# Performance work log

Hardware: AMD Instinct MI355X
Metric: run time of the kernel (lower is better)

## Reference

```python
import jax, jax.numpy as jnp
import numpy as np

SCALE = 64 ** -0.5
MAX_LR = 0.01


def newtonschulz5(t, steps=5, eps=1e-7, coefs=(3.4445, -4.775, 2.0315)):
    # t: [h, i, j]; orthogonalize via quintic Newton-Schulz iteration
    a, b, c = coefs
    should_transpose = t.shape[-2] > t.shape[-1]
    if should_transpose:
        t = jnp.swapaxes(t, -1, -2)
    norm = jnp.sqrt(jnp.sum(t * t, axis=(-1, -2), keepdims=True))
    t = t / jnp.maximum(norm, eps)
    for _ in range(steps):
        A = t @ jnp.swapaxes(t, -1, -2)
        B = b * A + c * (A @ A)
        t = a * t + B @ t
    if should_transpose:
        t = jnp.swapaxes(t, -1, -2)
    return t


def setup_inputs() -> dict:
    key = jax.random.key(0)
    ks = jax.random.split(key, 7)
    b, n, d, h, dh = 2, 2048, 512, 8, 64
    s = 0.05  # scale random weights for numerical sanity (softmax not one-hot)
    return {
        "tokens": jax.random.normal(ks[0], (b, n, d), jnp.float32),
        "rms_weight": jnp.ones((d,), jnp.float32),
        "wq": jax.random.normal(ks[1], (h, d, dh), jnp.float32) * s,
        "wk": jax.random.normal(ks[2], (h, d, dh), jnp.float32) * s,
        "wv": jax.random.normal(ks[3], (h, d, dh), jnp.float32) * s,
        "wo": jax.random.normal(ks[4], (h, dh, d), jnp.float32) * s,
        "lr_w": jax.random.normal(ks[5], (1, d), jnp.float32) * s,
        "tv_w": jax.random.normal(ks[6], (d, d), jnp.float32) * s,
        "return_next_memories": 1,
    }


def reference(tokens, rms_weight, wq, wk, wv, wo, lr_w, tv_w, return_next_memories):
    eps = jnp.finfo(tokens.dtype).eps
    # RMSNorm (torch nn.RMSNorm with eps=None -> finfo eps)
    t = tokens * jax.lax.rsqrt(jnp.mean(tokens * tokens, axis=-1, keepdims=True) + eps) * rms_weight

    q = jnp.einsum('bnd,hde->bhne', t, wq)  # [b,h,n,dh]
    k = jnp.einsum('bnd,hde->bhne', t, wk)
    v = jnp.einsum('bnd,hde->bhne', t, wv)

    score = jnp.einsum('bhie,bhje->bhij', q, k) * SCALE
    n = score.shape[-1]
    causal_mask = jnp.triu(jnp.ones((n, n), bool), 1)
    score = jnp.where(causal_mask, -jnp.finfo(score.dtype).max, score)
    attn = jax.nn.softmax(score, axis=-1)
    out = jnp.einsum('bhij,bhje->bhie', attn, v)  # [b,h,n,dh]
    pred_values = jnp.einsum('bhne,hed->bnd', out, wo)

    if not return_next_memories:
        return pred_values

    # target values: Linear(dim,dim,no bias) + LayerNorm(no affine) on shifted tokens
    tv = jnp.einsum('bnd,od->bno', t[:, 1:], tv_w)
    mu = jnp.mean(tv, axis=-1, keepdims=True)
    var = jnp.var(tv, axis=-1, keepdims=True)
    target_values = (tv - mu) * jax.lax.rsqrt(var + 1e-5)

    tok = t[:, :-1]                       # [b,n-1,d]
    pred_fw = pred_values[:, :-1]
    out_t = out[:, :, :-1]
    attn_t = attn[:, :, :-1, :-1]
    q_t, k_t, v_t = q[:, :, :-1], k[:, :, :-1], v[:, :, :-1]

    lr = jax.nn.sigmoid(jnp.einsum('bnd,od->bno', tok, lr_w)) * MAX_LR  # [b,n-1,1]
    error = (target_values - pred_fw) * lr

    dout = jnp.einsum('bnd,hed->bhne', error, wo)            # [b,h,n-1,dh]
    dwo = jnp.einsum('bnd,bhne->hed', error, out_t)          # [h,dh,d]
    delta = jnp.sum(dout * out_t, axis=-1, keepdims=True)    # [b,h,n-1,1]
    dv = jnp.einsum('bhij,bhie->bhje', attn_t, dout)
    dattn = jnp.einsum('bhje,bhie->bhij', v_t, dout)
    dscore = SCALE * attn_t * (dattn - delta)
    dq = jnp.einsum('bhje,bhij->bhie', k_t, dscore)
    dk = jnp.einsum('bhie,bhij->bhje', q_t, dscore)
    dwq = jnp.einsum('bhie,bid->hde', dq, tok)
    dwk = jnp.einsum('bhje,bjd->hde', dk, tok)
    dwv = jnp.einsum('bhje,bjd->hde', dv, tok)

    # muon update: Newton-Schulz orthogonalization of value/output fast-weight grads
    dwv = newtonschulz5(dwv)
    dwo = newtonschulz5(dwo)

    return (pred_values, dwq, dwk, dwv, dwo)
```

## Files before the change

### kernel.cpp

```cpp
#include <hip/hip_runtime.h>
#include <float.h>
#include <math.h>

#define B_   2
#define N_   2048
#define D_   512
#define H_   8
#define DH_  64
#define NM_  2047
#define SCALE_F 0.125f
#define LBK 72

typedef __attribute__((ext_vector_type(8))) short bf16x8;
typedef __attribute__((ext_vector_type(4))) float f32x4;
#define MFMA_B16(a,b,c) __builtin_amdgcn_mfma_f32_16x16x32_bf16(a,b,c,0,0,0)

__device__ __forceinline__ short f2bf(float f){
  unsigned u = __float_as_uint(f);
  unsigned r = u + 0x7fffu + ((u>>16)&1u);
  return (short)(r>>16);
}
__device__ __forceinline__ float bf2f(short s){
  return __uint_as_float(((unsigned)(unsigned short)s)<<16);
}
// ... 348 lines not shown
  s1=wred64(s1); s2=wred64(s2); s3=wred64(s3);
  __shared__ float r1[4],r2[4],r3[4];
  if((tid&63)==0){ int w=tid>>6; r1[w]=s1; r2[w]=s2; r3[w]=s3; }
  __syncthreads();
  float S1=r1[0]+r1[1]+r1[2]+r1[3];
  float S2=r2[0]+r2[1]+r2[2]+r2[3];
  float S3=r3[0]+r3[1]+r3[2]+r3[3];
  float mu  = S1*(1.f/512.f);
  float var = S2*(1.f/512.f) - mu*mu;
  float rstd= rsqrtf(var + 1e-5f);
  float lr  = 0.01f/(1.f+__expf(-S3));
  tv[tid]     = ((v0-mu)*rstd - pr[tid])*lr;
  tv[tid+256] = ((v1-mu)*rstd - pr[tid+256])*lr;
}

__global__ __launch_bounds__(256) void k_gemm_dout(const short* __restrict__ erb,
    const short* __restrict__ wob, short* __restrict__ doh, short* __restrict__ dot){
  __shared__ __attribute__((aligned(16))) short as[64][LBK], bs[64][LBK];
  int r0=blockIdx.x<<6, h=blockIdx.y;
  f32x4 acc[4];
  #pragma unroll
  for(int nb=0;nb<4;nb++) acc[nb]=(f32x4){0.f,0.f,0.f,0.f};
  gemm64(erb+(size_t)r0*512, 512, wob+(size_t)h*32768, 512, 8, as, bs, acc);
  int tid=threadIdx.x, w=tid>>6, lane=tid&63, lg=lane>>4, ln=lane&15;
  size_t bh=(size_t)(r0>>11)*8+h;
  int n0=(r0&2047)+w*16+lg*4;
  #pragma unroll
  for(int nb=0;nb<4;nb++){
    int e=nb*16+ln;
    short4 s4;
    s4.x=f2bf(acc[nb][0]); s4.y=f2bf(acc[nb][1]);
    s4.z=f2bf(acc[nb][2]); s4.w=f2bf(acc[nb][3]);
    doh[(bh*2048+n0  )*64+e]=s4.x;
    doh[(bh*2048+n0+1)*64+e]=s4.y;
    doh[(bh*2048+n0+2)*64+e]=s4.z;
    doh[(bh*2048+n0+3)*64+e]=s4.w;
    *(short4*)&dot[(bh*64+e)*2048+n0]=s4;
  }
}

__global__ __launch_bounds__(256) void k_delta(const short* __restrict__ doh,
    const short* __restrict__ obb, float* __restrict__ delta){
  int rid = blockIdx.x*4 + (threadIdx.x>>6);
  int lane = threadIdx.x&63;
  if(rid >= B_*H_*NM_) return;
  int b = rid/(H_*NM_); int rem = rid - b*H_*NM_;
  int h = rem/NM_; int i = rem - h*NM_;
  float v = bf2f(doh[((size_t)(b*H_+h)*N_ + i)*DH_ + lane])
          * bf2f(obb[((size_t)(b*N_+i))*D_ + h*DH_ + lane]);
  v = wred64(v);
  if(lane==0) delta[((size_t)(b*H_+h))*N_ + i] = v;
}

__global__ __launch_bounds__(256) void k_fa_dq(const short* __restrict__ qh,
    const short* __restrict__ kh, const short* __restrict__ vh,
    const short* __restrict__ kt, const short* __restrict__ doh,
    const float* __restrict__ lse, const float* __restrict__ delta,
    short* __restrict__ dqt, short* __restrict__ dqp1){
  int bh = blockIdx.x, it = blockIdx.y, half = blockIdx.z;
  int i0 = it<<6;
  const short* qhb = qh + (size_t)bh*N_*DH_;
  const short* khb = kh + (size_t)bh*N_*DH_;
  const short* vhb = vh + (size_t)bh*N_*DH_;
  const short* ktb = kt + (size_t)bh*DH_*N_;
  const short* dohb= doh+ (size_t)bh*N_*DH_;
  __shared__ __attribute__((aligned(16))) short ks[64][LBK], vs[64][LBK], kts[64][LBK];
  __shared__ __attribute__((aligned(16))) short psb[4][16][LBK];
  int tid=threadIdx.x, w=tid>>6, lane=tid&63, lg=lane>>4, ln=lane&15;
  bf16x8 aq[2], ad[2];
  float Lr[4], dl[4];
  #pragma unroll
  for(int s=0;s<2;s++){
    aq[s]=*(const bf16x8*)&qhb[(size_t)(i0+w*16+ln)*DH_+32*s+lg*8];
    ad[s]=*(const bf16x8*)&dohb[(size_t)(i0+w*16+ln)*DH_+32*s+lg*8];
  }
  #pragma unroll
  for(int r=0;r<4;r++){
    int ii=i0+w*16+lg*4+r;
    Lr[r]=lse[(size_t)bh*N_+ii];
    dl[r]=(ii<NM_)?delta[(size_t)bh*N_+ii]:0.f;
  }
  f32x4 acc[4];
  #pragma unroll
  for(int nb=0;nb<4;nb++) acc[nb]=(f32x4){0.f,0.f,0.f,0.f};
  int4 ka0,ka1,va0,va1,ta0,ta1;
  tload(khb+(size_t)half*64*DH_, DH_, tid, ka0,ka1);
  tload(vhb+(size_t)half*64*DH_, DH_, tid, va0,va1);
  tload(ktb+half*64, N_, tid, ta0,ta1);
  for(int jt=half;jt<=it;jt+=2){
    int j0=jt<<6;
    bool msk_needed = (jt==it) || (it==31);
    __syncthreads();
    twrite(ks, tid, ka0,ka1);
    twrite(vs, tid, va0,va1);
    twrite(kts, tid, ta0,ta1);
    if(jt+2<=it){
      tload(khb+(size_t)(jt+2)*64*DH_, DH_, tid, ka0,ka1);
      tload(vhb+(size_t)(jt+2)*64*DH_, DH_, tid, va0,va1);
      tload(ktb+(jt+2)*64, N_, tid, ta0,ta1);
    }
    __syncthreads();
    f32x4 sv[4], dav[4];
    __builtin_amdgcn_s_setprio(1);
    #pragma unroll
    for(int nb=0;nb<4;nb++){
      f32x4 z={0.f,0.f,0.f,0.f}, zd={0.f,0.f,0.f,0.f};
      #pragma unroll
      for(int s=0;s<2;s++){
        bf16x8 bk=*(const bf16x8*)&ks[nb*16+ln][32*s+lg*8];
        bf16x8 bv=*(const bf16x8*)&vs[nb*16+ln][32*s+lg*8];
        z = MFMA_B16(aq[s], bk, z);
        zd= MFMA_B16(ad[s], bv, zd);
      }
      sv[nb]=z; dav[nb]=zd;
    }
    __builtin_amdgcn_s_setprio(0);
    if(msk_needed){
      #pragma unroll
      for(int r=0;r<4;r++){
        int ii=i0+w*16+lg*4+r;
        #pragma unroll
        for(int nb=0;nb<4;nb++){
          int jj=j0+nb*16+ln;
          float pv=__expf(sv[nb][r]*SCALE_F - Lr[r]);
          float dsv=SCALE_F*pv*(dav[nb][r]-dl[r]);
          if(jj>ii || ii>=NM_ || jj>=NM_) dsv=0.f;
          psb[w][lg*4+r][ln+16*nb]=f2bf(dsv);
        }
      }
    } else {
      #pragma unroll
      for(int r=0;r<4;r++)
        #pragma unroll
        for(int nb=0;nb<4;nb++){
          float pv=__expf(sv[nb][r]*SCALE_F - Lr[r]);
          psb[w][lg*4+r][ln+16*nb]=f2bf(SCALE_F*pv*(dav[nb][r]-dl[r]));
        }
    }
    lds_fence();
    __builtin_amdgcn_s_setprio(1);
    #pragma unroll
    for(int nb=0;nb<4;nb++){
      #pragma unroll
      for(int s=0;s<2;s++){
        bf16x8 pa = *(const bf16x8*)&psb[w][ln][32*s+lg*8];
        bf16x8 bk = *(const bf16x8*)&kts[nb*16+ln][32*s+lg*8];
        acc[nb]=MFMA_B16(pa,bk,acc[nb]);
      }
    }
    __builtin_amdgcn_s_setprio(0);
    lds_fence();
  }
  short* dst = half? dqp1 : dqt;
  #pragma unroll
  for(int nb=0;nb<4;nb++){
    short4 s4;
    s4.x=f2bf(acc[nb][0]); s4.y=f2bf(acc[nb][1]);
    s4.z=f2bf(acc[nb][2]); s4.w=f2bf(acc[nb][3]);
    *(short4*)&dst[((size_t)bh*64 + nb*16+ln)*2048 + i0+w*16+lg*4]=s4;
  }
}

__global__ __launch_bounds__(256) void k_dqred(short* __restrict__ dqt,
    const short* __restrict__ dqp1){
  size_t i = ((size_t)blockIdx.x*256 + threadIdx.x)*8;
  int4 a = *(const int4*)&dqt[i];
  int4 b = *(const int4*)&dqp1[i];
  short* pa=(short*)&a; const short* pb=(const short*)&b;
  short out[8];
  #pragma unroll
  for(int k=0;k<8;k++) out[k]=f2bf(bf2f(pa[k])+bf2f(pb[k]));
  *(int4*)&dqt[i] = *(int4*)out;
}

__global__ __launch_bounds__(256) void k_fa_dkv(const short* __restrict__ kh,
    const short* __restrict__ vh, const short* __restrict__ qh,
    const short* __restrict__ qt, const short* __restrict__ doh,
    const short* __restrict__ dot,
    const float* __restrict__ lse, const float* __restrict__ delta,
    short* __restrict__ dkt, short* __restrict__ dvt,
    short* __restrict__ dkp1, short* __restrict__ dvp1){
  int bh = blockIdx.x, jt = blockIdx.y, half = blockIdx.z;
  int j0 = jt<<6;
  const short* khb = kh + (size_t)bh*N_*DH_;
  const short* vhb = vh + (size_t)bh*N_*DH_;
  const short* qhb = qh + (size_t)bh*N_*DH_;
  const short* qtb = qt + (size_t)bh*DH_*N_;
  const short* dohb= doh+ (size_t)bh*N_*DH_;
  const short* dotb= dot+ (size_t)bh*DH_*N_;
  __shared__ __attribute__((aligned(16))) short qs[64][LBK], dos[64][LBK], qts[64][LBK], dots[64][LBK];
  __shared__ __attribute__((aligned(16))) short ps[4][16][LBK];
  __shared__ float Ls[64], dls[64];
  int tid=threadIdx.x, w=tid>>6, lane=tid&63, lg=lane>>4, ln=lane&15;
  bf16x8 akf[2], avf[2];
  #pragma unroll
  for(int s=0;s<2;s++){
    akf[s]=*(const bf16x8*)&khb[(size_t)(j0+w*16+ln)*DH_+32*s+lg*8];
    avf[s]=*(const bf16x8*)&vhb[(size_t)(j0+w*16+ln)*DH_+32*s+lg*8];
  }
  f32x4 accv[4], acck[4];
  #pragma unroll
  for(int nb=0;nb<4;nb++){
    accv[nb]=(f32x4){0.f,0.f,0.f,0.f};
    acck[nb]=(f32x4){0.f,0.f,0.f,0.f};
  }
  int it0 = jt + half;
  int4 qa0,qa1,da0,da1,qta0,qta1,dta0,dta1;
  float Lnx=0.f, dlnx=0.f;
  {
    int ip = (it0<32)? (it0<<6) : 0;
    tload(qhb+(size_t)ip*DH_, DH_, tid, qa0,qa1);
    tload(dohb+(size_t)ip*DH_, DH_, tid, da0,da1);
    tload(qtb+ip, N_, tid, qta0,qta1);
    tload(dotb+ip, N_, tid, dta0,dta1);
    if(tid<64){
      int ii=ip+tid;
      Lnx=lse[(size_t)bh*N_+ii];
      dlnx=(ii<NM_)?delta[(size_t)bh*N_+ii]:0.f;
    }
  }
  for(int it=it0; it<32; it+=2){
    int i0=it<<6;
    bool msk_needed = (it==jt) || (it==31);
    __syncthreads();
    twrite(qs, tid, qa0,qa1);
    twrite(dos, tid, da0,da1);
    twrite(qts, tid, qta0,qta1);
    twrite(dots, tid, dta0,dta1);
    if(tid<64){ Ls[tid]=Lnx; dls[tid]=dlnx; }
    if(it+2<32){
      int i1=(it+2)<<6;
      tload(qhb+(size_t)i1*DH_, DH_, tid, qa0,qa1);
      tload(dohb+(size_t)i1*DH_, DH_, tid, da0,da1);
      tload(qtb+i1, N_, tid, qta0,qta1);
      tload(dotb+i1, N_, tid, dta0,dta1);
      if(tid<64){
        int ii=i1+tid;
        Lnx=lse[(size_t)bh*N_+ii];
        dlnx=(ii<NM_)?delta[(size_t)bh*N_+ii]:0.f;
      }
    }
    __syncthreads();
    f32x4 sv[4], dav[4];
    __builtin_amdgcn_s_setprio(1);
    #pragma unroll
    for(int nb=0;nb<4;nb++){
      f32x4 z={0.f,0.f,0.f,0.f}, zd={0.f,0.f,0.f,0.f};
      #pragma unroll
      for(int s=0;s<2;s++){
        bf16x8 bq=*(const bf16x8*)&qs[nb*16+ln][32*s+lg*8];
        bf16x8 bd=*(const bf16x8*)&dos[nb*16+ln][32*s+lg*8];
        z = MFMA_B16(akf[s], bq, z);
        zd= MFMA_B16(avf[s], bd, zd);
      }
      sv[nb]=z; dav[nb]=zd;
    }
    __builtin_amdgcn_s_setprio(0);
    float dsk[4][4];
    if(msk_needed){
      #pragma unroll
      for(int nb=0;nb<4;nb++){
        float Lc=Ls[nb*16+ln], dlc=dls[nb*16+ln];
        int ii=i0+nb*16+ln;
        #pragma unroll
        for(int r=0;r<4;r++){
          int jj=j0+w*16+lg*4+r;
          float pv=__expf(sv[nb][r]*SCALE_F - Lc);
          bool msk=(jj>ii)||(ii>=NM_)||(jj>=NM_);
          if(msk) pv=0.f;
          ps[w][lg*4+r][ln+16*nb]=f2bf(pv);
          dsk[nb][r]= msk?0.f: SCALE_F*pv*(dav[nb][r]-dlc);
        }
      }
    } else {
      #pragma unroll
      for(int nb=0;nb<4;nb++){
        float Lc=Ls[nb*16+ln], dlc=dls[nb*16+ln];
        #pragma unroll
        for(int r=0;r<4;r++){
          float pv=__expf(sv[nb][r]*SCALE_F - Lc);
          ps[w][lg*4+r][ln+16*nb]=f2bf(pv);
          dsk[nb][r]= SCALE_F*pv*(dav[nb][r]-dlc);
        }
      }
    }
    lds_fence();
    __builtin_amdgcn_s_setprio(1);
    #pragma unroll
    for(int nb=0;nb<4;nb++){
      #pragma unroll
      for(int s=0;s<2;s++){
        bf16x8 pa = *(const bf16x8*)&ps[w][ln][32*s+lg*8];
        bf16x8 bd = *(const bf16x8*)&dots[nb*16+ln][32*s+lg*8];
        accv[nb]=MFMA_B16(pa,bd,accv[nb]);
      }
    }
    __builtin_amdgcn_s_setprio(0);
    lds_fence();
    #pragma unroll
    for(int nb=0;nb<4;nb++)
      #pragma unroll
      for(int r=0;r<4;r++)
        ps[w][lg*4+r][ln+16*nb]=f2bf(dsk[nb][r]);
    lds_fence();
    __builtin_amdgcn_s_setprio(1);
    #pragma unroll
    for(int nb=0;nb<4;nb++){
      #pragma unroll
      for(int s=0;s<2;s++){
        bf16x8 pk = *(const bf16x8*)&ps[w][ln][32*s+lg*8];
        bf16x8 bq = *(const bf16x8*)&qts[nb*16+ln][32*s+lg*8];
        acck[nb]=MFMA_B16(pk,bq,acck[nb]);
      }
    }
    __builtin_amdgcn_s_setprio(0);
    lds_fence();
  }
  short* dvd = half? dvp1 : dvt;
  short* dkd = half? dkp1 : dkt;
  #pragma unroll
  for(int nb=0;nb<4;nb++){
    int e=nb*16+ln, n0=j0+w*16+lg*4;
    short4 s4;
    s4.x=f2bf(accv[nb][0]); s4.y=f2bf(accv[nb][1]);
    s4.z=f2bf(accv[nb][2]); s4.w=f2bf(accv[nb][3]);
    *(short4*)&dvd[((size_t)bh*64+e)*2048 + n0]=s4;
    s4.x=f2bf(acck[nb][0]); s4.y=f2bf(acck[nb][1]);
    s4.z=f2bf(acck[nb][2]); s4.w=f2bf(acck[nb][3]);
    *(short4*)&dkd[((size_t)bh*64+e)*2048 + n0]=s4;
  }
}

__global__ __launch_bounds__(256) void k_dkvred(short* __restrict__ dkt,
    short* __restrict__ dvt, const short* __restrict__ dkp1,
    const short* __restrict__ dvp1){
  int bid = blockIdx.x;
  short* dst; const short* src;
  if(bid<1024){ dst=dkt; src=dkp1; } else { dst=dvt; src=dvp1; bid-=1024; }
  size_t i = ((size_t)bid*256 + threadIdx.x)*8;
  int4 a = *(const int4*)&dst[i];
  int4 b = *(const int4*)&src[i];
  short* pa=(short*)&a; const short* pb=(const short*)&b;
  short out[8];
  #pragma unroll
  for(int k=0;k<8;k++) out[k]=f2bf(bf2f(pa[k])+bf2f(pb[k]));
  *(int4*)&dst[i] = *(int4*)out;
}

__global__ __launch_bounds__(256) void k_gemm_wgq(const short* __restrict__ tt,
    const short* __restrict__ g, float* __restrict__ par){
  __shared__ __attribute__((aligned(16))) short as[64][LBK], bs[64][LBK];
  int dt=blockIdx.x, h=blockIdx.y, sp=blockIdx.z;
  int b=sp>>2, n0b=(sp&3)*512;
  f32x4 acc[4];
  #pragma unroll
  for(int nb=0;nb<4;nb++) acc[nb]=(f32x4){0.f,0.f,0.f,0.f};
  gemm64(tt + (size_t)(dt*64)*4096 + sp*512, 4096,
         g  + ((size_t)(b*8+h)*64)*2048 + n0b, 2048, 8, as, bs, acc);
  int tid=threadIdx.x, w=tid>>6, lane=tid&63, lg=lane>>4, ln=lane&15;
  int row=w*16+lg*4;
  #pragma unroll
  for(int nb=0;nb<4;nb++)
    #pragma unroll
    for(int r=0;r<4;r++)
      par[(size_t)sp*262144 + (size_t)h*32768 + (size_t)(dt*64+row+r)*64 + nb*16+ln]=acc[nb][r];
}

__global__ __launch_bounds__(256) void k_gemm_wgo(const short* __restrict__ outt,
    const short* __restrict__ ert, float* __restrict__ par){
  __shared__ __attribute__((aligned(16))) short as[64][LBK], bs[64][LBK];
  int ct=blockIdx.x, h=blockIdx.y, sp=blockIdx.z;
  f32x4 acc[4];
  #pragma unroll
  for(int nb=0;nb<4;nb++) acc[nb]=(f32x4){0.f,0.f,0.f,0.f};
  gemm64(outt + (size_t)(h*64)*4096 + sp*512, 4096,
         ert  + (size_t)(ct*64)*4096 + sp*512, 4096, 8, as, bs, acc);
  int tid=threadIdx.x, w=tid>>6, lane=tid&63, lg=lane>>4, ln=lane&15;
  int row=w*16+lg*4;
  #pragma unroll
  for(int nb=0;nb<4;nb++)
    #pragma unroll
    for(int r=0;r<4;r++)
      par[(size_t)sp*262144 + (size_t)h*32768 + (size_t)(row+r)*512 + ct*64+nb*16+ln]=acc[nb][r];
}

__global__ __launch_bounds__(256) void k_wred_direct(const float* __restrict__ par,
    float* __restrict__ dst){
  int idx = blockIdx.x*256 + threadIdx.x;
  float s=0.f;
  #pragma unroll
  for(int sp=0;sp<8;sp++) s += par[(size_t)sp*262144 + idx];
  dst[idx]=s;
}
__global__ __launch_bounds__(256) void k_wred_xv(const float* __restrict__ par,
    float* __restrict__ X0){
  int idx = blockIdx.x*256 + threadIdx.x;
  float s=0.f;
  #pragma unroll
  for(int sp=0;sp<8;sp++) s += par[(size_t)sp*262144 + idx];
  int h=idx>>15, rem=idx&32767, d=rem>>6, e=rem&63;
  X0[(size_t)h*32768 + (size_t)e*512 + d]=s;
}
__global__ __launch_bounds__(256) void k_wred_xo(const float* __restrict__ par,
    float* __restrict__ X0){
  int idx = blockIdx.x*256 + threadIdx.x;
  float s=0.f;
  #pragma unroll
  for(int sp=0;sp<8;sp++) s += par[(size_t)sp*262144 + idx];
  X0[262144 + idx]=s;
}

__global__ __launch_bounds__(1024) void k_ns_fused(const float* __restrict__ X0,
    float* __restrict__ dwv, float* __restrict__ dwo){
  __shared__ __attribute__((aligned(16))) short Xl[64][520];
  __shared__ __attribute__((aligned(16))) short Xt[512][72];
  __shared__ __attribute__((aligned(16))) short Al[64][72];
  __shared__ __attribute__((aligned(16))) short Bl[64][72];
  __shared__ float red[16];
  int m = blockIdx.x, tid=threadIdx.x, w=tid>>6, lane=tid&63, lg=lane>>4, ln=lane&15;
  int wr=w>>2, wc=w&3;
  const float* Xg = X0 + (size_t)m*32768;
  float ss=0.f;
  for(int kk=0;kk<32;kk++){ float v=Xg[kk*1024+tid]; ss+=v*v; }
  ss=wred64(ss);
  if(lane==0) red[w]=ss;
  __syncthreads();
  float tot=0.f;
  #pragma unroll
  for(int i=0;i<16;i++) tot+=red[i];
  float sc = 1.f/fmaxf(sqrtf(tot), 1e-7f);
  for(int kk=0;kk<32;kk++){
    int idx=kk*1024+tid; int rr=idx>>9, cc=idx&511;
    short v=f2bf(Xg[idx]*sc);
    Xl[rr][cc]=v; Xt[cc][rr]=v;
  }
  __syncthreads();
  for(int iter=0; iter<5; ++iter){
    f32x4 accA=(f32x4){0.f,0.f,0.f,0.f};
    #pragma unroll
    for(int kt=0;kt<16;kt++){
      bf16x8 a = *(const bf16x8*)&Xl[wr*16+ln][kt*32+lg*8];
      bf16x8 b = *(const bf16x8*)&Xl[wc*16+ln][kt*32+lg*8];
      accA=MFMA_B16(a,b,accA);
    }
    #pragma unroll
    for(int r=0;r<4;r++) Al[wr*16+lg*4+r][wc*16+ln]=f2bf(accA[r]);
    __syncthreads();
    f32x4 acc2=(f32x4){0.f,0.f,0.f,0.f};
    #pragma unroll
    for(int s=0;s<2;s++){
      bf16x8 a = *(const bf16x8*)&Al[wr*16+ln][32*s+lg*8];
      bf16x8 b = *(const bf16x8*)&Al[wc*16+ln][32*s+lg*8];
      acc2=MFMA_B16(a,b,acc2);
    }
    #pragma unroll
    for(int r=0;r<4;r++)
      Bl[wr*16+lg*4+r][wc*16+ln]=f2bf(-4.775f*accA[r] + 2.0315f*acc2[r]);
    __syncthreads();
    int rg=(w&3)<<4, cg=(w>>2)<<7;
    f32x4 xn[8];
    #pragma unroll
    for(int nb=0;nb<8;nb++){
// ... 12 lines not shown
    if(iter<4){
      #pragma unroll
      for(int nb=0;nb<8;nb++){
        int d=cg+nb*16+ln, row0=rg+lg*4;
        short4 s4;
        s4.x=f2bf(xn[nb][0]); s4.y=f2bf(xn[nb][1]);
        s4.z=f2bf(xn[nb][2]); s4.w=f2bf(xn[nb][3]);
        Xl[row0  ][d]=s4.x; Xl[row0+1][d]=s4.y;
        Xl[row0+2][d]=s4.z; Xl[row0+3][d]=s4.w;
        *(short4*)&Xt[d][row0]=s4;
      }
      __syncthreads();
    } else {
      #pragma unroll
      for(int nb=0;nb<8;nb++){
        int d=cg+nb*16+ln, row0=rg+lg*4;
        #pragma unroll
        for(int r=0;r<4;r++){
          float v=xn[nb][r];
          int e=row0+r;
          if(m<8) dwv[(size_t)m*32768 + (size_t)d*64 + e]=v;
          else    dwo[(size_t)(m-8)*32768 + (size_t)e*512 + d]=v;
        }
      }
    }
  }
}

extern "C" void kernel_launch(void* const* d_in, const int* in_sizes, int n_in,
                              void* d_out, int out_size, void* d_ws, size_t ws_size,
                              hipStream_t stream) {
  const float* tokens=(const float*)d_in[0];
  const float* rmsw =(const float*)d_in[1];
  const float* wq   =(const float*)d_in[2];
  const float* wk   =(const float*)d_in[3];
  const float* wv   =(const float*)d_in[4];
  const float* wo   =(const float*)d_in[5];
  const float* lrw  =(const float*)d_in[6];
  const float* tvw  =(const float*)d_in[7];
  float* out = (float*)d_out;
  float* ws  = (float*)d_ws;

  short* tb   = (short*)(ws);
  short* tt   = (short*)(ws + 1064960);
  short* qh   = (short*)(ws + 2113536);
  short* kh   = (short*)(ws + 3162112);
  short* vh   = (short*)(ws + 4210688);
  short* qt   = (short*)(ws + 5259264);
  short* kt   = (short*)(ws + 6307840);
  short* vt   = (short*)(ws + 7356416);
  float* er_  = ws + 8404992;
  float* op0  = ws + 8404992;
  short* dqp1 = (short*)(ws + 8404992);
  short* dkp1 = (short*)(ws + 8404992);
  short* dvp1 = (short*)(ws + 9453568);
  short* obb  = (short*)(ws + 10502144);
  short* outt = (short*)(ws + 11550720);
  short* erb  = (short*)(ws + 12599296);
  short* ert  = (short*)(ws + 13647872);
  short* doh  = (short*)(ws + 14696448);
  short* dot  = (short*)(ws + 15745024);
  float* par_ = ws + 14696448;
  float* op1  = ws + 14696448;
  short* dqt  = (short*)(ws + 16793600);
  float* mlb  = ws + 16793600;
  short* dkt  = (short*)(ws + 17842176);
  short* dvt  = (short*)(ws + 18890752);
  short* wqt  = (short*)(ws + 19939328);
  short* wkt  = (short*)(ws + 20070400);
  short* wvt  = (short*)(ws + 20201472);
  short* wob  = (short*)(ws + 20332544);
  short* wot  = (short*)(ws + 20463616);
  short* tvwb = (short*)(ws + 20594688);
  float* lse_ = ws + 20725760;
  float* dlt_ = ws + 20758528;
  float* X0_  = ws + 20791296;

  float* OUT_PRED = out;
  float* OUT_DWQ  = out + 2097152;
  float* OUT_DWK  = out + 2359296;
  float* OUT_DWV  = out + 2621440;
  float* OUT_DWO  = out + 2883584;

  k_rmsnorm<<<4160,256,0,stream>>>(tokens, rmsw, tb);
  k_wprep<<<272,256,0,stream>>>(wq,wk,wv,wo,tvw, wqt,wkt,wvt,wob,wot,tvwb);
  k_gemm_qkv<<<dim3(64,24),256,0,stream>>>(tb, wqt,wkt,wvt, qh,kh,vh, qt,kt,vt);
  k_fa_fwd<<<dim3(16,32,2),256,0,stream>>>(qh, kh, vt, op0, op1, mlb);
  k_fa_merge<<<8192,256,0,stream>>>(op0, op1, mlb, obb, lse_);
  k_gemm_pred<<<dim3(64,8),256,0,stream>>>(obb, wot, OUT_PRED);

  if(out_size < 3145728) return;

  k_trans_b<<<dim3(64,8),256,0,stream>>>(tb, tt);
  k_gemm_tv<<<dim3(64,8),256,0,stream>>>(tb, tvwb, er_);
  k_lnerr<<<4094,256,0,stream>>>(er_, tb, OUT_PRED, lrw);
  k_trans_f<<<dim3(64,8),256,0,stream>>>(er_, erb, ert);
  k_gemm_dout<<<dim3(64,8),256,0,stream>>>(erb, wob, doh, dot);
  k_delta<<<8188,256,0,stream>>>(doh, obb, dlt_);
  k_fa_dq<<<dim3(16,32,2),256,0,stream>>>(qh, kh, vh, kt, doh, lse_, dlt_, dqt, dqp1);
  k_dqred<<<1024,256,0,stream>>>(dqt, dqp1);
  k_fa_dkv<<<dim3(16,32,2),256,0,stream>>>(kh, vh, qh, qt, doh, dot, lse_, dlt_,
                                           dkt, dvt, dkp1, dvp1);
  k_dkvred<<<2048,256,0,stream>>>(dkt, dvt, dkp1, dvp1);
  k_trans_b<<<dim3(64,8),256,0,stream>>>(obb, outt);

  k_gemm_wgq<<<dim3(8,8,8),256,0,stream>>>(tt, dqt, par_);
  k_wred_direct<<<1024,256,0,stream>>>(par_, OUT_DWQ);
  k_gemm_wgq<<<dim3(8,8,8),256,0,stream>>>(tt, dkt, par_);
  k_wred_direct<<<1024,256,0,stream>>>(par_, OUT_DWK);
  k_gemm_wgq<<<dim3(8,8,8),256,0,stream>>>(tt, dvt, par_);
  k_wred_xv<<<1024,256,0,stream>>>(par_, X0_);
  k_gemm_wgo<<<dim3(8,8,8),256,0,stream>>>(outt, ert, par_);
  k_wred_xo<<<1024,256,0,stream>>>(par_, X0_);

  k_ns_fused<<<16,1024,0,stream>>>(X0_, OUT_DWV, OUT_DWO);
}
```

Measured before the change: 311.5 us.

## Merge attention backward dq and dkv kernels and batch weight-grad GEMMs into single launches

Combines the dq and dk/dv flash-attention backward kernels into one launch, with the z-index choosing the role. Their split-half reductions are merged into one reduction kernel. The four weight-gradient GEMMs and their reductions are also batched into single launches, writing to separate partial buffers carved from reused workspace. This removes many kernel launches and tail-underfill gaps and lets independent work run concurrently, at the cost of a larger merged kernel (LDS sized for the dkv path) and workspace aliasing that must not overlap live data.

```diff
diff --git a/kernel.cpp b/kernel.cpp
--- a/kernel.cpp
+++ b/kernel.cpp
@@ -424,291 +424,273 @@
   if(lane==0) delta[((size_t)(b*H_+h))*N_ + i] = v;
 }
 
-__global__ __launch_bounds__(256) void k_fa_dq(const short* __restrict__ qh,
+__global__ __launch_bounds__(256) void k_fa_bwd(const short* __restrict__ qh,
     const short* __restrict__ kh, const short* __restrict__ vh,
-    const short* __restrict__ kt, const short* __restrict__ doh,
+    const short* __restrict__ qt, const short* __restrict__ kt,
+    const short* __restrict__ doh, const short* __restrict__ dot,
     const float* __restrict__ lse, const float* __restrict__ delta,
-    short* __restrict__ dqt, short* __restrict__ dqp1){
-  int bh = blockIdx.x, it = blockIdx.y, half = blockIdx.z;
-  int i0 = it<<6;
+    short* __restrict__ dqt, short* __restrict__ dqp1,
+    short* __restrict__ dkt, short* __restrict__ dvt,
+    short* __restrict__ dkp1, short* __restrict__ dvp1){
+  __shared__ __attribute__((aligned(16))) short t0[64][LBK], t1[64][LBK], t2[64][LBK], t3[64][LBK];
+  __shared__ __attribute__((aligned(16))) short ps[4][16][LBK];
+  __shared__ float Ls[64], dls[64];
+  int bh = blockIdx.x, tid=threadIdx.x, w=tid>>6, lane=tid&63, lg=lane>>4, ln=lane&15;
   const short* qhb = qh + (size_t)bh*N_*DH_;
   const short* khb = kh + (size_t)bh*N_*DH_;
   const short* vhb = vh + (size_t)bh*N_*DH_;
+  const short* qtb = qt + (size_t)bh*DH_*N_;
   const short* ktb = kt + (size_t)bh*DH_*N_;
   const short* dohb= doh+ (size_t)bh*N_*DH_;
-  __shared__ __attribute__((aligned(16))) short ks[64][LBK], vs[64][LBK], kts[64][LBK];
-  __shared__ __attribute__((aligned(16))) short psb[4][16][LBK];
-  int tid=threadIdx.x, w=tid>>6, lane=tid&63, lg=lane>>4, ln=lane&15;
-  bf16x8 aq[2], ad[2];
-  float Lr[4], dl[4];
-  #pragma unroll
-  for(int s=0;s<2;s++){
-    aq[s]=*(const bf16x8*)&qhb[(size_t)(i0+w*16+ln)*DH_+32*s+lg*8];
-    ad[s]=*(const bf16x8*)&dohb[(size_t)(i0+w*16+ln)*DH_+32*s+lg*8];
-  }
-  #pragma unroll
-  for(int r=0;r<4;r++){
-    int ii=i0+w*16+lg*4+r;
-    Lr[r]=lse[(size_t)bh*N_+ii];
-    dl[r]=(ii<NM_)?delta[(size_t)bh*N_+ii]:0.f;
-  }
-  f32x4 acc[4];
-  #pragma unroll
-  for(int nb=0;nb<4;nb++) acc[nb]=(f32x4){0.f,0.f,0.f,0.f};
-  int4 ka0,ka1,va0,va1,ta0,ta1;
-  tload(khb+(size_t)half*64*DH_, DH_, tid, ka0,ka1);
-  tload(vhb+(size_t)half*64*DH_, DH_, tid, va0,va1);
-  tload(ktb+half*64, N_, tid, ta0,ta1);
-  for(int jt=half;jt<=it;jt+=2){
-    int j0=jt<<6;
-    bool msk_needed = (jt==it) || (it==31);
-    __syncthreads();
-    twrite(ks, tid, ka0,ka1);
-    twrite(vs, tid, va0,va1);
-    twrite(kts, tid, ta0,ta1);
-    if(jt+2<=it){
-      tload(khb+(size_t)(jt+2)*64*DH_, DH_, tid, ka0,ka1);
-      tload(vhb+(size_t)(jt+2)*64*DH_, DH_, tid, va0,va1);
-      tload(ktb+(jt+2)*64, N_, tid, ta0,ta1);
-    }
-    __syncthreads();
-    f32x4 sv[4], dav[4];
-    __builtin_amdgcn_s_setprio(1);
+  const short* dotb= dot+ (size_t)bh*DH_*N_;
+
+  if(blockIdx.z < 2){
+    int it = blockIdx.y, half = blockIdx.z;
+    int i0 = it<<6;
+    bf16x8 aq[2], ad[2];
+    float Lr[4], dl[4];
+    #pragma unroll
+    for(int s=0;s<2;s++){
+      aq[s]=*(const bf16x8*)&qhb[(size_t)(i0+w*16+ln)*DH_+32*s+lg*8];
+      ad[s]=*(const bf16x8*)&dohb[(size_t)(i0+w*16+ln)*DH_+32*s+lg*8];
+    }
+    #pragma unroll
+    for(int r=0;r<4;r++){
+      int ii=i0+w*16+lg*4+r;
+      Lr[r]=lse[(size_t)bh*N_+ii];
+      dl[r]=(ii<NM_)?delta[(size_t)bh*N_+ii]:0.f;
+    }
+    f32x4 acc[4];
+    #pragma unroll
+    for(int nb=0;nb<4;nb++) acc[nb]=(f32x4){0.f,0.f,0.f,0.f};
+    int4 ka0,ka1,va0,va1,ta0,ta1;
+    tload(khb+(size_t)half*64*DH_, DH_, tid, ka0,ka1);
+    tload(vhb+(size_t)half*64*DH_, DH_, tid, va0,va1);
+    tload(ktb+half*64, N_, tid, ta0,ta1);
+    for(int jt=half;jt<=it;jt+=2){
+      int j0=jt<<6;
+      bool msk_needed = (jt==it) || (it==31);
+      __syncthreads();
+      twrite(t0, tid, ka0,ka1);
+      twrite(t1, tid, va0,va1);
+      twrite(t2, tid, ta0,ta1);
+      if(jt+2<=it){
+        tload(khb+(size_t)(jt+2)*64*DH_, DH_, tid, ka0,ka1);
+        tload(vhb+(size_t)(jt+2)*64*DH_, DH_, tid, va0,va1);
+        tload(ktb+(jt+2)*64, N_, tid, ta0,ta1);
+      }
+      __syncthreads();
+      f32x4 sv[4], dav[4];
+      __builtin_amdgcn_s_setprio(1);
+      #pragma unroll
+      for(int nb=0;nb<4;nb++){
+        f32x4 z={0.f,0.f,0.f,0.f}, zd={0.f,0.f,0.f,0.f};
+        #pragma unroll
+        for(int s=0;s<2;s++){
+          bf16x8 bk=*(const bf16x8*)&t0[nb*16+ln][32*s+lg*8];
+          bf16x8 bv=*(const bf16x8*)&t1[nb*16+ln][32*s+lg*8];
+          z = MFMA_B16(aq[s], bk, z);
+          zd= MFMA_B16(ad[s], bv, zd);
+        }
+        sv[nb]=z; dav[nb]=zd;
+      }
+      __builtin_amdgcn_s_setprio(0);
+      if(msk_needed){
+        #pragma unroll
+        for(int r=0;r<4;r++){
+          int ii=i0+w*16+lg*4+r;
+          #pragma unroll
+          for(int nb=0;nb<4;nb++){
+            int jj=j0+nb*16+ln;
+            float pv=__expf(sv[nb][r]*SCALE_F - Lr[r]);
+            float dsv=SCALE_F*pv*(dav[nb][r]-dl[r]);
+            if(jj>ii || ii>=NM_ || jj>=NM_) dsv=0.f;
+            ps[w][lg*4+r][ln+16*nb]=f2bf(dsv);
+          }
+        }
+      } else {
+        #pragma unroll
+        for(int r=0;r<4;r++)
+          #pragma unroll
+          for(int nb=0;nb<4;nb++){
+            float pv=__expf(sv[nb][r]*SCALE_F - Lr[r]);
+            ps[w][lg*4+r][ln+16*nb]=f2bf(SCALE_F*pv*(dav[nb][r]-dl[r]));
+          }
+      }
+      lds_fence();
+      __builtin_amdgcn_s_setprio(1);
+      #pragma unroll
+      for(int nb=0;nb<4;nb++){
+        #pragma unroll
+        for(int s=0;s<2;s++){
+          bf16x8 pa = *(const bf16x8*)&ps[w][ln][32*s+lg*8];
+          bf16x8 bk = *(const bf16x8*)&t2[nb*16+ln][32*s+lg*8];
+          acc[nb]=MFMA_B16(pa,bk,acc[nb]);
+        }
+      }
+      __builtin_amdgcn_s_setprio(0);
+      lds_fence();
+    }
+    short* dst = half? dqp1 : dqt;
     #pragma unroll
     for(int nb=0;nb<4;nb++){
-      f32x4 z={0.f,0.f,0.f,0.f}, zd={0.f,0.f,0.f,0.f};
-      #pragma unroll
-      for(int s=0;s<2;s++){
-        bf16x8 bk=*(const bf16x8*)&ks[nb*16+ln][32*s+lg*8];
-        bf16x8 bv=*(const bf16x8*)&vs[nb*16+ln][32*s+lg*8];
-        z = MFMA_B16(aq[s], bk, z);
-        zd= MFMA_B16(ad[s], bv, zd);
-      }
-      sv[nb]=z; dav[nb]=zd;
-    }
-    __builtin_amdgcn_s_setprio(0);
-    if(msk_needed){
-      #pragma unroll
-      for(int r=0;r<4;r++){
-        int ii=i0+w*16+lg*4+r;
-        #pragma unroll
-        for(int nb=0;nb<4;nb++){
-          int jj=j0+nb*16+ln;
-          float pv=__expf(sv[nb][r]*SCALE_F - Lr[r]);
-          float dsv=SCALE_F*pv*(dav[nb][r]-dl[r]);
-          if(jj>ii || ii>=NM_ || jj>=NM_) dsv=0.f;
-          psb[w][lg*4+r][ln+16*nb]=f2bf(dsv);
-        }
-      }
-    } else {
-      #pragma unroll
-      for(int r=0;r<4;r++)
-        #pragma unroll
-        for(int nb=0;nb<4;nb++){
-          float pv=__expf(sv[nb][r]*SCALE_F - Lr[r]);
-          psb[w][lg*4+r][ln+16*nb]=f2bf(SCALE_F*pv*(dav[nb][r]-dl[r]));
-        }
-    }
-    lds_fence();
-    __builtin_amdgcn_s_setprio(1);
+      short4 s4;
+      s4.x=f2bf(acc[nb][0]); s4.y=f2bf(acc[nb][1]);
+      s4.z=f2bf(acc[nb][2]); s4.w=f2bf(acc[nb][3]);
+      *(short4*)&dst[((size_t)bh*64 + nb*16+ln)*2048 + i0+w*16+lg*4]=s4;
+    }
+  } else {
+    int jt = blockIdx.y, half = blockIdx.z-2;
+    int j0 = jt<<6;
+    bf16x8 akf[2], avf[2];
+    #pragma unroll
+    for(int s=0;s<2;s++){
+      akf[s]=*(const bf16x8*)&khb[(size_t)(j0+w*16+ln)*DH_+32*s+lg*8];
+      avf[s]=*(const bf16x8*)&vhb[(size_t)(j0+w*16+ln)*DH_+32*s+lg*8];
+    }
+    f32x4 accv[4], acck[4];
     #pragma unroll
     for(int nb=0;nb<4;nb++){
-      #pragma unroll
-      for(int s=0;s<2;s++){
-        bf16x8 pa = *(const bf16x8*)&psb[w][ln][32*s+lg*8];
-        bf16x8 bk = *(const bf16x8*)&kts[nb*16+ln][32*s+lg*8];
-        acc[nb]=MFMA_B16(pa,bk,acc[nb]);
-      }
-    }
-    __builtin_amdgcn_s_setprio(0);
-    lds_fence();
-  }
-  short* dst = half? dqp1 : dqt;
-  #pragma unroll
-  for(int nb=0;nb<4;nb++){
-    short4 s4;
-    s4.x=f2bf(acc[nb][0]); s4.y=f2bf(acc[nb][1]);
-    s4.z=f2bf(acc[nb][2]); s4.w=f2bf(acc[nb][3]);
-    *(short4*)&dst[((size_t)bh*64 + nb*16+ln)*2048 + i0+w*16+lg*4]=s4;
-  }
-}
-
-__global__ __launch_bounds__(256) void k_dqred(short* __restrict__ dqt,
-    const short* __restrict__ dqp1){
-  size_t i = ((size_t)blockIdx.x*256 + threadIdx.x)*8;
-  int4 a = *(const int4*)&dqt[i];
-  int4 b = *(const int4*)&dqp1[i];
-  short* pa=(short*)&a; const short* pb=(const short*)&b;
-  short out[8];
-  #pragma unroll
-  for(int k=0;k<8;k++) out[k]=f2bf(bf2f(pa[k])+bf2f(pb[k]));
-  *(int4*)&dqt[i] = *(int4*)out;
-}
-
-__global__ __launch_bounds__(256) void k_fa_dkv(const short* __restrict__ kh,
-    const short* __restrict__ vh, const short* __restrict__ qh,
-    const short* __restrict__ qt, const short* __restrict__ doh,
-    const short* __restrict__ dot,
-    const float* __restrict__ lse, const float* __restrict__ delta,
-    short* __restrict__ dkt, short* __restrict__ dvt,
-    short* __restrict__ dkp1, short* __restrict__ dvp1){
-  int bh = blockIdx.x, jt = blockIdx.y, half = blockIdx.z;
-  int j0 = jt<<6;
-  const short* khb = kh + (size_t)bh*N_*DH_;
-  const short* vhb = vh + (size_t)bh*N_*DH_;
-  const short* qhb = qh + (size_t)bh*N_*DH_;
-  const short* qtb = qt + (size_t)bh*DH_*N_;
-  const short* dohb= doh+ (size_t)bh*N_*DH_;
-  const short* dotb= dot+ (size_t)bh*DH_*N_;
-  __shared__ __attribute__((aligned(16))) short qs[64][LBK], dos[64][LBK], qts[64][LBK], dots[64][LBK];
-  __shared__ __attribute__((aligned(16))) short ps[4][16][LBK];
-  __shared__ float Ls[64], dls[64];
-  int tid=threadIdx.x, w=tid>>6, lane=tid&63, lg=lane>>4, ln=lane&15;
-  bf16x8 akf[2], avf[2];
-  #pragma unroll
-  for(int s=0;s<2;s++){
-    akf[s]=*(const bf16x8*)&khb[(size_t)(j0+w*16+ln)*DH_+32*s+lg*8];
-    avf[s]=*(const bf16x8*)&vhb[(size_t)(j0+w*16+ln)*DH_+32*s+lg*8];
-  }
-  f32x4 accv[4], acck[4];
-  #pragma unroll
-  for(int nb=0;nb<4;nb++){
-    accv[nb]=(f32x4){0.f,0.f,0.f,0.f};
-    acck[nb]=(f32x4){0.f,0.f,0.f,0.f};
-  }
-  int it0 = jt + half;
-  int4 qa0,qa1,da0,da1,qta0,qta1,dta0,dta1;
-  float Lnx=0.f, dlnx=0.f;
-  {
-    int ip = (it0<32)? (it0<<6) : 0;
-    tload(qhb+(size_t)ip*DH_, DH_, tid, qa0,qa1);
-    tload(dohb+(size_t)ip*DH_, DH_, tid, da0,da1);
-    tload(qtb+ip, N_, tid, qta0,qta1);
-    tload(dotb+ip, N_, tid, dta0,dta1);
-    if(tid<64){
-      int ii=ip+tid;
-      Lnx=lse[(size_t)bh*N_+ii];
-      dlnx=(ii<NM_)?delta[(size_t)bh*N_+ii]:0.f;
-    }
-  }
-  for(int it=it0; it<32; it+=2){
-    int i0=it<<6;
-    bool msk_needed = (it==jt) || (it==31);
-    __syncthreads();
-    twrite(qs, tid, qa0,qa1);
-    twrite(dos, tid, da0,da1);
-    twrite(qts, tid, qta0,qta1);
-    twrite(dots, tid, dta0,dta1);
-    if(tid<64){ Ls[tid]=Lnx; dls[tid]=dlnx; }
-    if(it+2<32){
-      int i1=(it+2)<<6;
-      tload(qhb+(size_t)i1*DH_, DH_, tid, qa0,qa1);
-      tload(dohb+(size_t)i1*DH_, DH_, tid, da0,da1);
-      tload(qtb+i1, N_, tid, qta0,qta1);
-      tload(dotb+i1, N_, tid, dta0,dta1);
+      accv[nb]=(f32x4){0.f,0.f,0.f,0.f};
+      acck[nb]=(f32x4){0.f,0.f,0.f,0.f};
+    }
+    int it0 = jt + half;
+    int4 qa0,qa1,da0,da1,qta0,qta1,dta0,dta1;
+    float Lnx=0.f, dlnx=0.f;
+    {
+      int ip = (it0<32)? (it0<<6) : 0;
+      tload(qhb+(size_t)ip*DH_, DH_, tid, qa0,qa1);
+      tload(dohb+(size_t)ip*DH_, DH_, tid, da0,da1);
+      tload(qtb+ip, N_, tid, qta0,qta1);
+      tload(dotb+ip, N_, tid, dta0,dta1);
       if(tid<64){
-        int ii=i1+tid;
+        int ii=ip+tid;
         Lnx=lse[(size_t)bh*N_+ii];
         dlnx=(ii<NM_)?delta[(size_t)bh*N_+ii]:0.f;
       }
     }
-    __syncthreads();
-    f32x4 sv[4], dav[4];
-    __builtin_amdgcn_s_setprio(1);
+    for(int it=it0; it<32; it+=2){
+      int i0=it<<6;
+      bool msk_needed = (it==jt) || (it==31);
+      __syncthreads();
+      twrite(t0, tid, qa0,qa1);
+      twrite(t1, tid, da0,da1);
+      twrite(t2, tid, qta0,qta1);
+      twrite(t3, tid, dta0,dta1);
+      if(tid<64){ Ls[tid]=Lnx; dls[tid]=dlnx; }
+      if(it+2<32){
+        int i1=(it+2)<<6;
+        tload(qhb+(size_t)i1*DH_, DH_, tid, qa0,qa1);
+        tload(dohb+(size_t)i1*DH_, DH_, tid, da0,da1);
+        tload(qtb+i1, N_, tid, qta0,qta1);
+        tload(dotb+i1, N_, tid, dta0,dta1);
+        if(tid<64){
+          int ii=i1+tid;
+          Lnx=lse[(size_t)bh*N_+ii];
+          dlnx=(ii<NM_)?delta[(size_t)bh*N_+ii]:0.f;
+        }
+      }
+      __syncthreads();
+      f32x4 sv[4], dav[4];
+      __builtin_amdgcn_s_setprio(1);
+      #pragma unroll
+      for(int nb=0;nb<4;nb++){
+        f32x4 z={0.f,0.f,0.f,0.f}, zd={0.f,0.f,0.f,0.f};
+        #pragma unroll
+        for(int s=0;s<2;s++){
+          bf16x8 bq=*(const bf16x8*)&t0[nb*16+ln][32*s+lg*8];
+          bf16x8 bd=*(const bf16x8*)&t1[nb*16+ln][32*s+lg*8];
+          z = MFMA_B16(akf[s], bq, z);
+          zd= MFMA_B16(avf[s], bd, zd);
+        }
+        sv[nb]=z; dav[nb]=zd;
+      }
+      __builtin_amdgcn_s_setprio(0);
+      float dsk[4][4];
+      if(msk_needed){
+        #pragma unroll
+        for(int nb=0;nb<4;nb++){
+          float Lc=Ls[nb*16+ln], dlc=dls[nb*16+ln];
+          int ii=i0+nb*16+ln;
+          #pragma unroll
+          for(int r=0;r<4;r++){
+            int jj=j0+w*16+lg*4+r;
+            float pv=__expf(sv[nb][r]*SCALE_F - Lc);
+            bool msk=(jj>ii)||(ii>=NM_)||(jj>=NM_);
+            if(msk) pv=0.f;
+            ps[w][lg*4+r][ln+16*nb]=f2bf(pv);
+            dsk[nb][r]= msk?0.f: SCALE_F*pv*(dav[nb][r]-dlc);
+          }
+        }
+      } else {
+        #pragma unroll
+        for(int nb=0;nb<4;nb++){
+          float Lc=Ls[nb*16+ln], dlc=dls[nb*16+ln];
+          #pragma unroll
+          for(int r=0;r<4;r++){
+            float pv=__expf(sv[nb][r]*SCALE_F - Lc);
+            ps[w][lg*4+r][ln+16*nb]=f2bf(pv);
+            dsk[nb][r]= SCALE_F*pv*(dav[nb][r]-dlc);
+          }
+        }
+      }
+      lds_fence();
+      __builtin_amdgcn_s_setprio(1);
+      #pragma unroll
+      for(int nb=0;nb<4;nb++){
+        #pragma unroll
+        for(int s=0;s<2;s++){
+          bf16x8 pa = *(const bf16x8*)&ps[w][ln][32*s+lg*8];
+          bf16x8 bd = *(const bf16x8*)&t3[nb*16+ln][32*s+lg*8];
+          accv[nb]=MFMA_B16(pa,bd,accv[nb]);
+        }
+      }
+      __builtin_amdgcn_s_setprio(0);
+      lds_fence();
+      #pragma unroll
+      for(int nb=0;nb<4;nb++)
+        #pragma unroll
+        for(int r=0;r<4;r++)
+          ps[w][lg*4+r][ln+16*nb]=f2bf(dsk[nb][r]);
+      lds_fence();
+      __builtin_amdgcn_s_setprio(1);
+      #pragma unroll
+      for(int nb=0;nb<4;nb++){
+        #pragma unroll
+        for(int s=0;s<2;s++){
+          bf16x8 pk = *(const bf16x8*)&ps[w][ln][32*s+lg*8];
+          bf16x8 bq = *(const bf16x8*)&t2[nb*16+ln][32*s+lg*8];
+          acck[nb]=MFMA_B16(pk,bq,acck[nb]);
+        }
+      }
+      __builtin_amdgcn_s_setprio(0);
+      lds_fence();
+    }
+    short* dvd = half? dvp1 : dvt;
+    short* dkd = half? dkp1 : dkt;
     #pragma unroll
     for(int nb=0;nb<4;nb++){
-      f32x4 z={0.f,0.f,0.f,0.f}, zd={0.f,0.f,0.f,0.f};
-      #pragma unroll
-      for(int s=0;s<2;s++){
-        bf16x8 bq=*(const bf16x8*)&qs[nb*16+ln][32*s+lg*8];
-        bf16x8 bd=*(const bf16x8*)&dos[nb*16+ln][32*s+lg*8];
-        z = MFMA_B16(akf[s], bq, z);
-        zd= MFMA_B16(avf[s], bd, zd);
-      }
-      sv[nb]=z; dav[nb]=zd;
-    }
-    __builtin_amdgcn_s_setprio(0);
-    float dsk[4][4];
-    if(msk_needed){
-      #pragma unroll
-      for(int nb=0;nb<4;nb++){
-        float Lc=Ls[nb*16+ln], dlc=dls[nb*16+ln];
-        int ii=i0+nb*16+ln;
-        #pragma unroll
-        for(int r=0;r<4;r++){
-          int jj=j0+w*16+lg*4+r;
-          float pv=__expf(sv[nb][r]*SCALE_F - Lc);
-          bool msk=(jj>ii)||(ii>=NM_)||(jj>=NM_);
-          if(msk) pv=0.f;
-          ps[w][lg*4+r][ln+16*nb]=f2bf(pv);
-          dsk[nb][r]= msk?0.f: SCALE_F*pv*(dav[nb][r]-dlc);
-        }
-      }
-    } else {
-      #pragma unroll
-      for(int nb=0;nb<4;nb++){
-        float Lc=Ls[nb*16+ln], dlc=dls[nb*16+ln];
-        #pragma unroll
-        for(int r=0;r<4;r++){
-          float pv=__expf(sv[nb][r]*SCALE_F - Lc);
-          ps[w][lg*4+r][ln+16*nb]=f2bf(pv);
-          dsk[nb][r]= SCALE_F*pv*(dav[nb][r]-dlc);
-        }
-      }
-    }
-    lds_fence();
-    __builtin_amdgcn_s_setprio(1);
-    #pragma unroll
-    for(int nb=0;nb<4;nb++){
-      #pragma unroll
-      for(int s=0;s<2;s++){
-        bf16x8 pa = *(const bf16x8*)&ps[w][ln][32*s+lg*8];
-        bf16x8 bd = *(const bf16x8*)&dots[nb*16+ln][32*s+lg*8];
-        accv[nb]=MFMA_B16(pa,bd,accv[nb]);
-      }
-    }
-    __builtin_amdgcn_s_setprio(0);
-    lds_fence();
-    #pragma unroll
-    for(int nb=0;nb<4;nb++)
-      #pragma unroll
-      for(int r=0;r<4;r++)
-        ps[w][lg*4+r][ln+16*nb]=f2bf(dsk[nb][r]);
-    lds_fence();
-    __builtin_amdgcn_s_setprio(1);
-    #pragma unroll
-    for(int nb=0;nb<4;nb++){
-      #pragma unroll
-      for(int s=0;s<2;s++){
-        bf16x8 pk = *(const bf16x8*)&ps[w][ln][32*s+lg*8];
-        bf16x8 bq = *(const bf16x8*)&qts[nb*16+ln][32*s+lg*8];
-        acck[nb]=MFMA_B16(pk,bq,acck[nb]);
-      }
-    }
-    __builtin_amdgcn_s_setprio(0);
-    lds_fence();
-  }
-  short* dvd = half? dvp1 : dvt;
-  short* dkd = half? dkp1 : dkt;
-  #pragma unroll
-  for(int nb=0;nb<4;nb++){
-    int e=nb*16+ln, n0=j0+w*16+lg*4;
-    short4 s4;
-    s4.x=f2bf(accv[nb][0]); s4.y=f2bf(accv[nb][1]);
-    s4.z=f2bf(accv[nb][2]); s4.w=f2bf(accv[nb][3]);
-    *(short4*)&dvd[((size_t)bh*64+e)*2048 + n0]=s4;
-    s4.x=f2bf(acck[nb][0]); s4.y=f2bf(acck[nb][1]);
-    s4.z=f2bf(acck[nb][2]); s4.w=f2bf(acck[nb][3]);
-    *(short4*)&dkd[((size_t)bh*64+e)*2048 + n0]=s4;
-  }
-}
-
-__global__ __launch_bounds__(256) void k_dkvred(short* __restrict__ dkt,
-    short* __restrict__ dvt, const short* __restrict__ dkp1,
+      int e=nb*16+ln, n0=j0+w*16+lg*4;
+      short4 s4;
+      s4.x=f2bf(accv[nb][0]); s4.y=f2bf(accv[nb][1]);
+      s4.z=f2bf(accv[nb][2]); s4.w=f2bf(accv[nb][3]);
+      *(short4*)&dvd[((size_t)bh*64+e)*2048 + n0]=s4;
+      s4.x=f2bf(acck[nb][0]); s4.y=f2bf(acck[nb][1]);
+      s4.z=f2bf(acck[nb][2]); s4.w=f2bf(acck[nb][3]);
+      *(short4*)&dkd[((size_t)bh*64+e)*2048 + n0]=s4;
+    }
+  }
+}
+
+__global__ __launch_bounds__(256) void k_dred(short* __restrict__ dqt,
+    short* __restrict__ dkt, short* __restrict__ dvt,
+    const short* __restrict__ dqp1, const short* __restrict__ dkp1,
     const short* __restrict__ dvp1){
   int bid = blockIdx.x;
   short* dst; const short* src;
-  if(bid<1024){ dst=dkt; src=dkp1; } else { dst=dvt; src=dvp1; bid-=1024; }
+  if(bid<1024){ dst=dqt; src=dqp1; }
+  else if(bid<2048){ dst=dkt; src=dkp1; bid-=1024; }
+  else { dst=dvt; src=dvp1; bid-=2048; }
   size_t i = ((size_t)bid*256 + threadIdx.x)*8;
   int4 a = *(const int4*)&dst[i];
   int4 b = *(const int4*)&src[i];
@@ -719,67 +701,59 @@
   *(int4*)&dst[i] = *(int4*)out;
 }
 
-__global__ __launch_bounds__(256) void k_gemm_wgq(const short* __restrict__ tt,
-    const short* __restrict__ g, float* __restrict__ par){
+__global__ __launch_bounds__(256) void k_gemm_wg(const short* __restrict__ tt,
+    const short* __restrict__ dqt, const short* __restrict__ dkt,
+    const short* __restrict__ dvt, const short* __restrict__ outt,
+    const short* __restrict__ ert,
+    float* __restrict__ pA, float* __restrict__ pB,
+    float* __restrict__ pC, float* __restrict__ pD){
   __shared__ __attribute__((aligned(16))) short as[64][LBK], bs[64][LBK];
-  int dt=blockIdx.x, h=blockIdx.y, sp=blockIdx.z;
-  int b=sp>>2, n0b=(sp&3)*512;
+  int x=blockIdx.x, h=blockIdx.y, z=blockIdx.z;
+  int sp=z&7, which=z>>3;
   f32x4 acc[4];
   #pragma unroll
   for(int nb=0;nb<4;nb++) acc[nb]=(f32x4){0.f,0.f,0.f,0.f};
-  gemm64(tt + (size_t)(dt*64)*4096 + sp*512, 4096,
-         g  + ((size_t)(b*8+h)*64)*2048 + n0b, 2048, 8, as, bs, acc);
   int tid=threadIdx.x, w=tid>>6, lane=tid&63, lg=lane>>4, ln=lane&15;
   int row=w*16+lg*4;
-  #pragma unroll
-  for(int nb=0;nb<4;nb++)
-    #pragma unroll
-    for(int r=0;r<4;r++)
-      par[(size_t)sp*262144 + (size_t)h*32768 + (size_t)(dt*64+row+r)*64 + nb*16+ln]=acc[nb][r];
-}
-
-__global__ __launch_bounds__(256) void k_gemm_wgo(const short* __restrict__ outt,
-    const short* __restrict__ ert, float* __restrict__ par){
-  __shared__ __attribute__((aligned(16))) short as[64][LBK], bs[64][LBK];
-  int ct=blockIdx.x, h=blockIdx.y, sp=blockIdx.z;
-  f32x4 acc[4];
-  #pragma unroll
-  for(int nb=0;nb<4;nb++) acc[nb]=(f32x4){0.f,0.f,0.f,0.f};
-  gemm64(outt + (size_t)(h*64)*4096 + sp*512, 4096,
-         ert  + (size_t)(ct*64)*4096 + sp*512, 4096, 8, as, bs, acc);
-  int tid=threadIdx.x, w=tid>>6, lane=tid&63, lg=lane>>4, ln=lane&15;
-  int row=w*16+lg*4;
-  #pragma unroll
-  for(int nb=0;nb<4;nb++)
-    #pragma unroll
-    for(int r=0;r<4;r++)
-      par[(size_t)sp*262144 + (size_t)h*32768 + (size_t)(row+r)*512 + ct*64+nb*16+ln]=acc[nb][r];
-}
-
-__global__ __launch_bounds__(256) void k_wred_direct(const float* __restrict__ par,
-    float* __restrict__ dst){
-  int idx = blockIdx.x*256 + threadIdx.x;
+  if(which<3){
+    const short* g = which==0? dqt : which==1? dkt : dvt;
+    float* par = which==0? pA : which==1? pB : pC;
+    int b=sp>>2, n0b=(sp&3)*512;
+    gemm64(tt + (size_t)(x*64)*4096 + sp*512, 4096,
+           g  + ((size_t)(b*8+h)*64)*2048 + n0b, 2048, 8, as, bs, acc);
+    #pragma unroll
+    for(int nb=0;nb<4;nb++)
+      #pragma unroll
+      for(int r=0;r<4;r++)
+        par[(size_t)sp*262144 + (size_t)h*32768 + (size_t)(x*64+row+r)*64 + nb*16+ln]=acc[nb][r];
+  } else {
+    gemm64(outt + (size_t)(h*64)*4096 + sp*512, 4096,
+           ert  + (size_t)(x*64)*4096 + sp*512, 4096, 8, as, bs, acc);
+    #pragma unroll
+    for(int nb=0;nb<4;nb++)
+      #pragma unroll
+      for(int r=0;r<4;r++)
+        pD[(size_t)sp*262144 + (size_t)h*32768 + (size_t)(row+r)*512 + x*64+nb*16+ln]=acc[nb][r];
+  }
+}
+
+__global__ __launch_bounds__(256) void k_wred(const float* __restrict__ pA,
+    const float* __restrict__ pB, const float* __restrict__ pC,
+    const float* __restrict__ pD, float* __restrict__ dwq,
+    float* __restrict__ dwk, float* __restrict__ X0){
+  int bid = blockIdx.x;
+  int grp = bid>>10;
+  int idx = (bid&1023)*256 + threadIdx.x;
+  const float* par = grp==0? pA : grp==1? pB : grp==2? pC : pD;
   float s=0.f;
   #pragma unroll
   for(int sp=0;sp<8;sp++) s += par[(size_t)sp*262144 + idx];
-  dst[idx]=s;
-}
-__global__ __launch_bounds__(256) void k_wred_xv(const float* __restrict__ par,
-    float* __restrict__ X0){
-  int idx = blockIdx.x*256 + threadIdx.x;
-  float s=0.f;
-  #pragma unroll
-  for(int sp=0;sp<8;sp++) s += par[(size_t)sp*262144 + idx];
-  int h=idx>>15, rem=idx&32767, d=rem>>6, e=rem&63;
-  X0[(size_t)h*32768 + (size_t)e*512 + d]=s;
-}
-__global__ __launch_bounds__(256) void k_wred_xo(const float* __restrict__ par,
-    float* __restrict__ X0){
-  int idx = blockIdx.x*256 + threadIdx.x;
-  float s=0.f;
-  #pragma unroll
-  for(int sp=0;sp<8;sp++) s += par[(size_t)sp*262144 + idx];
-  X0[262144 + idx]=s;
+  if(grp==0) dwq[idx]=s;
+  else if(grp==1) dwk[idx]=s;
+  else if(grp==2){
+    int h=idx>>15, rem=idx&32767, d=rem>>6, e=rem&63;
+    X0[(size_t)h*32768 + (size_t)e*512 + d]=s;
+  } else X0[262144 + idx]=s;
 }
 
 __global__ __launch_bounds__(1024) void k_ns_fused(const float* __restrict__ X0,
@@ -898,20 +872,23 @@
   float* er_  = ws + 8404992;
   float* op0  = ws + 8404992;
   short* dqp1 = (short*)(ws + 8404992);
-  short* dkp1 = (short*)(ws + 8404992);
   short* dvp1 = (short*)(ws + 9453568);
   short* obb  = (short*)(ws + 10502144);
+  short* dkp1 = (short*)(ws + 10502144);
   short* outt = (short*)(ws + 11550720);
   short* erb  = (short*)(ws + 12599296);
   short* ert  = (short*)(ws + 13647872);
   short* doh  = (short*)(ws + 14696448);
   short* dot  = (short*)(ws + 15745024);
-  float* par_ = ws + 14696448;
   float* op1  = ws + 14696448;
+  float* parD = ws + 14696448;
   short* dqt  = (short*)(ws + 16793600);
   float* mlb  = ws + 16793600;
   short* dkt  = (short*)(ws + 17842176);
   short* dvt  = (short*)(ws + 18890752);
+  float* parA = ws + 2113536;
+  float* parB = ws + 4210688;
+  float* parC = ws + 6307840;
   short* wqt  = (short*)(ws + 19939328);
   short* wkt  = (short*)(ws + 20070400);
   short* wvt  = (short*)(ws + 20201472);
@@ -943,21 +920,15 @@
   k_trans_f<<<dim3(64,8),256,0,stream>>>(er_, erb, ert);
   k_gemm_dout<<<dim3(64,8),256,0,stream>>>(erb, wob, doh, dot);
   k_delta<<<8188,256,0,stream>>>(doh, obb, dlt_);
-  k_fa_dq<<<dim3(16,32,2),256,0,stream>>>(qh, kh, vh, kt, doh, lse_, dlt_, dqt, dqp1);
-  k_dqred<<<1024,256,0,stream>>>(dqt, dqp1);
-  k_fa_dkv<<<dim3(16,32,2),256,0,stream>>>(kh, vh, qh, qt, doh, dot, lse_, dlt_,
+  k_trans_b<<<dim3(64,8),256,0,stream>>>(obb, outt);
+  k_fa_bwd<<<dim3(16,32,4),256,0,stream>>>(qh, kh, vh, qt, kt, doh, dot,
+                                           lse_, dlt_, dqt, dqp1,
                                            dkt, dvt, dkp1, dvp1);
-  k_dkvred<<<2048,256,0,stream>>>(dkt, dvt, dkp1, dvp1);
-  k_trans_b<<<dim3(64,8),256,0,stream>>>(obb, outt);
-
-  k_gemm_wgq<<<dim3(8,8,8),256,0,stream>>>(tt, dqt, par_);
-  k_wred_direct<<<1024,256,0,stream>>>(par_, OUT_DWQ);
-  k_gemm_wgq<<<dim3(8,8,8),256,0,stream>>>(tt, dkt, par_);
-  k_wred_direct<<<1024,256,0,stream>>>(par_, OUT_DWK);
-  k_gemm_wgq<<<dim3(8,8,8),256,0,stream>>>(tt, dvt, par_);
-  k_wred_xv<<<1024,256,0,stream>>>(par_, X0_);
-  k_gemm_wgo<<<dim3(8,8,8),256,0,stream>>>(outt, ert, par_);
-  k_wred_xo<<<1024,256,0,stream>>>(par_, X0_);
+  k_dred<<<3072,256,0,stream>>>(dqt, dkt, dvt, dqp1, dkp1, dvp1);
+
+  k_gemm_wg<<<dim3(8,8,32),256,0,stream>>>(tt, dqt, dkt, dvt, outt, ert,
+                                           parA, parB, parC, parD);
+  k_wred<<<4096,256,0,stream>>>(parA, parB, parC, parD, OUT_DWQ, OUT_DWK, X0_);
 
   k_ns_fused<<<16,1024,0,stream>>>(X0_, OUT_DWV, OUT_DWO);
 }
```

After: 293.2 us. 1.06x faster.
